# Optimization experiments

Measured on AMD Instinct MI355X. Metric: run time of the kernel, lower is better.

The kernel has to match this reference:

```python
import jax, jax.numpy as jnp
import numpy as np

H_IMG = 128; W_IMG = 128
TANFOVX = 0.5; TANFOVY = 0.5
SCALE_MOD = 1.0
C0 = 0.28209479177387814
C1 = 0.4886025119029199
C2 = (1.0925484305920792, -1.0925484305920792, 0.31539156525252005, -1.0925484305920792, 0.5462742152960396)
C3 = (-0.5900435899266435, 2.890611442640554, -0.4570457994644658, 0.3731763325901154, -0.4570457994644658, 1.445305721320277, -0.5900435899266435)


def quat_to_rot(q):
    q = q / jnp.linalg.norm(q, axis=-1, keepdims=True)
    r, x, y, z = q[..., 0], q[..., 1], q[..., 2], q[..., 3]
    row0 = jnp.stack([1 - 2 * (y * y + z * z), 2 * (x * y - r * z), 2 * (x * z + r * y)], -1)
    row1 = jnp.stack([2 * (x * y + r * z), 1 - 2 * (x * x + z * z), 2 * (y * z - r * x)], -1)
    row2 = jnp.stack([2 * (x * z - r * y), 2 * (y * z + r * x), 1 - 2 * (x * x + y * y)], -1)
    return jnp.stack([row0, row1, row2], -2)  # [P,3,3]


def eval_sh(sh, d):
    # sh: [P,16,3], d: [P,3] unit view directions -> RGB per gaussian (degree 3)
    x, y, z = d[:, 0:1], d[:, 1:2], d[:, 2:3]
    res = C0 * sh[:, 0]
    res = res - C1 * y * sh[:, 1] + C1 * z * sh[:, 2] - C1 * x * sh[:, 3]
    xx, yy, zz = x * x, y * y, z * z
    xy, yz, xz = x * y, y * z, x * z
    res = (res + C2[0] * xy * sh[:, 4] + C2[1] * yz * sh[:, 5]
           + C2[2] * (2 * zz - xx - yy) * sh[:, 6] + C2[3] * xz * sh[:, 7]
           + C2[4] * (xx - yy) * sh[:, 8])
    res = (res + C3[0] * y * (3 * xx - yy) * sh[:, 9] + C3[1] * xy * z * sh[:, 10]
           + C3[2] * y * (4 * zz - xx - yy) * sh[:, 11]
           + C3[3] * z * (2 * zz - 3 * xx - 3 * yy) * sh[:, 12]
           + C3[4] * x * (4 * zz - xx - yy) * sh[:, 13]
           + C3[5] * z * (xx - yy) * sh[:, 14] + C3[6] * x * (xx - 3 * yy) * sh[:, 15])
    return jnp.maximum(res + 0.5, 0.0)


def _render_one(means, sh, opac, scales, rots, bg, target, view, proj, campos):
    P = means.shape[0]
    fx = W_IMG / (2.0 * TANFOVX)
    fy = H_IMG / (2.0 * TANFOVY)
    ones = jnp.ones((P, 1), means.dtype)
    xyz1 = jnp.concatenate([means, ones], axis=1)
    hom = xyz1 @ proj.T                                   # [P,4]
    p_w = 1.0 / (hom[:, 3] + 1e-7)
    p_proj = hom[:, :3] * p_w[:, None]
    p_view = xyz1 @ view.T
    depth = p_view[:, 2]
    in_front = depth > 0.2

    # 3D covariance: Sigma = R diag(s) (R diag(s))^T
    R = quat_to_rot(rots)
    M = R * (scales * SCALE_MOD)[:, None, :]
    Sigma = M @ jnp.swapaxes(M, 1, 2)                     # [P,3,3]

    # EWA Jacobian -> 2D covariance
    tz = depth
    txc = jnp.clip(p_view[:, 0] / tz, -1.3 * TANFOVX, 1.3 * TANFOVX) * tz
    tyc = jnp.clip(p_view[:, 1] / tz, -1.3 * TANFOVY, 1.3 * TANFOVY) * tz
    zp = jnp.zeros_like(tz)
    J = jnp.stack([jnp.stack([fx / tz, zp, -fx * txc / (tz * tz)], -1),
                   jnp.stack([zp, fy / tz, -fy * tyc / (tz * tz)], -1)], -2)  # [P,2,3]
    T = J @ view[:3, :3]
    cov2d = T @ Sigma @ jnp.swapaxes(T, 1, 2)             # [P,2,2]
    c00 = cov2d[:, 0, 0] + 0.3
    c11 = cov2d[:, 1, 1] + 0.3
    c01 = cov2d[:, 0, 1]
    det = c00 * c11 - c01 * c01
    valid = in_front & (det > 1e-12)
    inv_det = 1.0 / jnp.where(det > 1e-12, det, 1.0)
    conic = jnp.stack([c11 * inv_det, -c01 * inv_det, c00 * inv_det], -1)
    mid = 0.5 * (c00 + c11)
    lam = mid + jnp.sqrt(jnp.maximum(mid * mid - det, 0.1))
    radii = jnp.where(valid, jnp.ceil(3.0 * jnp.sqrt(lam)), 0.0)

    # NDC -> pixel centers
    px = ((p_proj[:, 0] + 1.0) * W_IMG - 1.0) * 0.5
    py = ((p_proj[:, 1] + 1.0) * H_IMG - 1.0) * 0.5

    dirs = means - campos[None]
    dirs = dirs / jnp.linalg.norm(dirs, axis=-1, keepdims=True)
    colors = eval_sh(sh, dirs)                            # [P,3]

    # front-to-back depth order (same per-pixel order as the tile sort)
    order = jnp.argsort(depth)
    inv_order = jnp.argsort(order)
    px_s, py_s = px[order], py[order]
    con_s = conic[order]
    col_s = colors[order]
    op_s = opac[order, 0]
    val_s = valid[order]

    xs = jnp.arange(W_IMG, dtype=means.dtype)
    ys = jnp.arange(H_IMG, dtype=means.dtype)
    dx = px_s[:, None, None] - xs[None, None, :]          # [P,1,W] -> [P,H,W]
    dy = py_s[:, None, None] - ys[None, :, None]
    power = (-0.5 * (con_s[:, 0, None, None] * dx * dx + con_s[:, 2, None, None] * dy * dy)
             - con_s[:, 1, None, None] * dx * dy)         # [P,H,W]
    alpha = jnp.minimum(0.99, op_s[:, None, None] * jnp.exp(jnp.minimum(power, 0.0)))
    keep = (power <= 0.0) & (alpha >= 1.0 / 255.0) & val_s[:, None, None]
    alpha = jnp.where(keep, alpha, 0.0)
    trans = jnp.cumprod(1.0 - alpha, axis=0)
    T_exc = jnp.concatenate([jnp.ones((1, H_IMG, W_IMG), alpha.dtype), trans[:-1]], axis=0)
    w = alpha * T_exc                                     # per-gaussian pixel weights
    T_final = trans[-1]
    color = jnp.einsum('phw,pc->chw', w, col_s) + T_final[None] * bg[:, None, None]
    alpha_img = (1.0 - T_final)[None]
    est_color = jnp.einsum('phw,chw->pc', w, target)[inv_order]
    est_weight = w.sum(axis=(1, 2))[inv_order, None]
    return color, alpha_img, est_color, est_weight, radii


def reference(means3D, sh, opacities, scales, rotations, target_image, bg, viewmatrix, projmatrix, campos):
    f = jax.vmap(_render_one, in_axes=(0, 0, 0, 0, 0, 0, 0, None, None, None))
    return f(means3D, sh, opacities, scales, rotations, bg, target_image, viewmatrix, projmatrix, campos)


def setup_inputs() -> dict:
    key = jax.random.key(0)
    ks = jax.random.split(key, 8)
    B, P, K = 2, 1024, 16
    xy = jax.random.normal(ks[0], (B, P, 2), jnp.float32) * 1.5
    z = jax.random.uniform(ks[1], (B, P, 1), jnp.float32, 2.0, 6.0)
    means3D = jnp.concatenate([xy, z], -1)
    sh = jax.random.normal(ks[2], (B, P, K, 3), jnp.float32) * 0.3
    opacities = jax.random.uniform(ks[3], (B, P, 1), jnp.float32)
    scales = jax.random.uniform(ks[4], (B, P, 3), jnp.float32, 0.01, 0.08)
    rotations = jax.random.normal(ks[5], (B, P, 4), jnp.float32)
    target_image = jax.random.uniform(ks[6], (B, 3, H_IMG, W_IMG), jnp.float32)
    bg = jax.random.uniform(ks[7], (B, 3), jnp.float32)
    view = np.eye(4, dtype=np.float32)  # camera at origin, +z forward
    znear, zfar = 0.01, 100.0
    proj = np.zeros((4, 4), np.float32)
    proj[0, 0] = 1.0 / TANFOVX
    proj[1, 1] = 1.0 / TANFOVY
    proj[2, 2] = zfar / (zfar - znear)
    proj[2, 3] = -(zfar * znear) / (zfar - znear)
    proj[3, 2] = 1.0
    return {"means3D": means3D, "sh": sh, "opacities": opacities, "scales": scales,
            "rotations": rotations, "target_image": target_image, "bg": bg,
            "viewmatrix": jnp.asarray(view), "projmatrix": jnp.asarray(proj @ view),
            "campos": jnp.zeros((3,), jnp.float32)}
```

## Files before the change

kernel.cpp:

```cpp
#include <hip/hip_runtime.h>
#include <math.h>

#define HI 128
#define WI 128
#define BB 2
#define PG 1024
#define NE (BB*PG)
#define NTILES 128
#define NRED 16
#define MAGIC_HI 0xFEEDFACECAFE0000ULL
#define MASK_HI  0xFFFFFFFFFFFF0000ULL

#define OFF_ALPHA (BB*3*HI*WI)
#define OFF_ESTC  (OFF_ALPHA + BB*HI*WI)
#define OFF_ESTW  (OFF_ESTC + BB*PG*3)
#define OFF_RADII (OFF_ESTW + BB*PG)

struct PC {
  float px, py, ex, ey;
  float A, B, C, op;
  unsigned key;
  float radii;
};

__device__ __forceinline__ PC proj_cull(int e,
    const float* __restrict__ means, const float* __restrict__ opac,
    const float* __restrict__ scales, const float* __restrict__ rots,
    const float* __restrict__ vm, const float* __restrict__ pm)
{
  PC o;
  float mx = means[e*3+0], my = means[e*3+1], mz = means[e*3+2];

  float hom0 = pm[0]*mx + pm[1]*my + pm[2]*mz + pm[3];
  float hom1 = pm[4]*mx + pm[5]*my + pm[6]*mz + pm[7];
  float hom3 = pm[12]*mx + pm[13]*my + pm[14]*mz + pm[15];
  float p_w  = 1.0f / (hom3 + 1e-7f);
  float pp0 = hom0 * p_w, pp1 = hom1 * p_w;

  float pv0   = vm[0]*mx + vm[1]*my + vm[2]*mz  + vm[3];
  float pv1   = vm[4]*mx + vm[5]*my + vm[6]*mz  + vm[7];
  float depth = vm[8]*mx + vm[9]*my + vm[10]*mz + vm[11];

  float qr = rots[e*4+0], qx = rots[e*4+1], qy = rots[e*4+2], qz = rots[e*4+3];
  float qn = sqrtf(qr*qr + qx*qx + qy*qy + qz*qz);
  qr /= qn; qx /= qn; qy /= qn; qz /= qn;
  float R00 = 1.0f-2.0f*(qy*qy+qz*qz), R01 = 2.0f*(qx*qy-qr*qz), R02 = 2.0f*(qx*qz+qr*qy);
  float R10 = 2.0f*(qx*qy+qr*qz), R11 = 1.0f-2.0f*(qx*qx+qz*qz), R12 = 2.0f*(qy*qz-qr*qx);
  float R20 = 2.0f*(qx*qz-qr*qy), R21 = 2.0f*(qy*qz+qr*qx), R22 = 1.0f-2.0f*(qx*qx+qy*qy);

  float s0 = scales[e*3+0], s1 = scales[e*3+1], s2 = scales[e*3+2];
  float M00=R00*s0, M01=R01*s1, M02=R02*s2;
  float M10=R10*s0, M11=R11*s1, M12=R12*s2;
  float M20=R20*s0, M21=R21*s1, M22=R22*s2;
  float S00 = M00*M00+M01*M01+M02*M02;
  float S01 = M00*M10+M01*M11+M02*M12;
  float S02 = M00*M20+M01*M21+M02*M22;
  float S11 = M10*M10+M11*M11+M12*M12;
  float S12 = M10*M20+M11*M21+M12*M22;
  float S22 = M20*M20+M21*M21+M22*M22;

  const float fx = 128.0f, fyc = 128.0f;
  float tz = depth;
  float txc = fminf(fmaxf(pv0/tz, -0.65f), 0.65f) * tz;
  float tyc = fminf(fmaxf(pv1/tz, -0.65f), 0.65f) * tz;
  float J00 = fx/tz,  J02 = -fx*txc/(tz*tz);
  float J11 = fyc/tz, J12 = -fyc*tyc/(tz*tz);

  float T00 = J00*vm[0] + J02*vm[8];
  float T01 = J00*vm[1] + J02*vm[9];
  float T02 = J00*vm[2] + J02*vm[10];
  float T10 = J11*vm[4] + J12*vm[8];
  float T11 = J11*vm[5] + J12*vm[9];
  float T12 = J11*vm[6] + J12*vm[10];

  float TS00 = T00*S00 + T01*S01 + T02*S02;
  float TS01 = T00*S01 + T01*S11 + T02*S12;
  float TS02 = T00*S02 + T01*S12 + T02*S22;
  float TS10 = T10*S00 + T11*S01 + T12*S02;
  float TS11 = T10*S01 + T11*S11 + T12*S12;
  float TS12 = T10*S02 + T11*S12 + T12*S22;

  float c00 = TS00*T00 + TS01*T01 + TS02*T02 + 0.3f;
  float c01 = TS00*T10 + TS01*T11 + TS02*T12;
  float c11 = TS10*T10 + TS11*T11 + TS12*T12 + 0.3f;

  float det = c00*c11 - c01*c01;
  bool valid = (depth > 0.2f) && (det > 1e-12f);
  float inv_det = 1.0f / (det > 1e-12f ? det : 1.0f);
  o.A =  c11 * inv_det;
  o.B = -c01 * inv_det;
  o.C =  c00 * inv_det;
  float mid = 0.5f * (c00 + c11);
  float lam = mid + sqrtf(fmaxf(mid*mid - det, 0.1f));
  o.radii = valid ? ceilf(3.0f * sqrtf(lam)) : 0.0f;

  o.px = ((pp0 + 1.0f)*WI - 1.0f)*0.5f;
  o.py = ((pp1 + 1.0f)*HI - 1.0f)*0.5f;

  float opv = opac[e];
  o.op = opv;
  float tau = logf(255.0f * opv);
  bool rok = valid && (tau > 0.0f);
  o.ex = rok ? sqrtf(2.0f*tau*c00) + 0.02f : -1e9f;
  o.ey = rok ? sqrtf(2.0f*tau*c11) + 0.02f : -1e9f;

  unsigned u = __float_as_uint(depth);
  o.key = (u >> 31) ? ~u : (u | 0x80000000u);
  return o;
}

__device__ __forceinline__ void sh_color(int e,
    const float* __restrict__ sh, const float* __restrict__ means,
    const float* __restrict__ campos, float col[3])
{
  float mx = means[e*3+0], my = means[e*3+1], mz = means[e*3+2];
  float dxr = mx - campos[0], dyr = my - campos[1], dzr = mz - campos[2];
  float dn = sqrtf(dxr*dxr + dyr*dyr + dzr*dzr);
  float x = dxr/dn, y = dyr/dn, z = dzr/dn;
  float xx=x*x, yy=y*y, zz=z*z, xy=x*y, yz=y*z, xz=x*z;
  const float* S = sh + e*48;
  #pragma unroll
  for (int c = 0; c < 3; ++c) {
    float r = 0.28209479177387814f * S[0+c];
    r -= 0.4886025119029199f * y * S[3+c];
    r += 0.4886025119029199f * z * S[6+c];
    r -= 0.4886025119029199f * x * S[9+c];
    r += 1.0925484305920792f  * xy * S[12+c];
    r += -1.0925484305920792f * yz * S[15+c];
    r += 0.31539156525252005f * (2.0f*zz-xx-yy) * S[18+c];
    r += -1.0925484305920792f * xz * S[21+c];
    r += 0.5462742152960396f  * (xx-yy) * S[24+c];
    r += -0.5900435899266435f * y * (3.0f*xx-yy) * S[27+c];
    r += 2.890611442640554f   * xy * z * S[30+c];
    r += -0.4570457994644658f * y * (4.0f*zz-xx-yy) * S[33+c];
    r += 0.3731763325901154f  * z * (2.0f*zz-3.0f*xx-3.0f*yy) * S[36+c];
    r += -0.4570457994644658f * x * (4.0f*zz-xx-yy) * S[39+c];
    r += 1.445305721320277f   * z * (xx-yy) * S[42+c];
    r += -0.5900435899266435f * x * (xx-3.0f*yy) * S[45+c];
    col[c] = fmaxf(r + 0.5f, 0.0f);
  }
}

__global__ __launch_bounds__(256) void fused_kernel(
    const float* __restrict__ means, const float* __restrict__ sh,
    const float* __restrict__ opac, const float* __restrict__ scales,
    const float* __restrict__ rots, const float* __restrict__ vm,
    const float* __restrict__ pm, const float* __restrict__ campos,
    const float* __restrict__ target, const float* __restrict__ bg,
    float4* __restrict__ pval, unsigned long long* __restrict__ flags,
    int* __restrict__ pgid, float* __restrict__ out)
{
  const int t = threadIdx.x;
  const int blk = blockIdx.x;

  __shared__ unsigned long long skey[PG];
  __shared__ float4 recA[256], recB[256], colC[256], stgt[256];
  __shared__ float  wmat[32][264];
  __shared__ int    scount;
  __shared__ int    scnt[64], soff[65];

  if (blk < NTILES) {
    const int b = blk >> 6, tile = blk & 63;
    const int tx0i = (tile & 7) * 16, ty0i = (tile >> 3) * 16;
    const int xi = tx0i + (t & 15), yi = ty0i + (t >> 4);
    const float fxp = (float)xi, fyp = (float)yi;
    const float rx0 = (float)tx0i, ry0 = (float)ty0i;

    if (t == 0) scount = 0;
    stgt[t] = make_float4(target[((b*3+0)*HI + yi)*WI + xi],
                          target[((b*3+1)*HI + yi)*WI + xi],
                          target[((b*3+2)*HI + yi)*WI + xi], 1.0f);
    __syncthreads();

    for (int k = 0; k < 4; ++k) {
      int ci = k*256 + t;
      PC r = proj_cull((b<<10)+ci, means, opac, scales, rots, vm, pm);
      bool ok = (r.px + r.ex >= rx0) && (r.px - r.ex <= rx0 + 15.0f)
             && (r.py + r.ey >= ry0) && (r.py - r.ey <= ry0 + 15.0f);
      if (ok) {
        int pos = atomicAdd(&scount, 1);
        skey[pos] = (((unsigned long long)r.key) << 10) | (unsigned)ci;
      }
    }
    __syncthreads();
    int total = scount;

    if (total > 1) {
      if (total <= 64) {
        if (t < 64) {
          unsigned long long v = (t < total) ? skey[t] : ~0ull;
          #pragma unroll
          for (int k = 2; k <= 64; k <<= 1) {
            bool dirAsc = ((t & k) == 0);
            #pragma unroll
            for (int j = k >> 1; j > 0; j >>= 1) {
              unsigned long long o = __shfl_xor(v, j, 64);
              bool takeMin = (((t & j) == 0) == dirAsc);
              bool less = v < o;
              v = (takeMin == less) ? v : o;
            }
          }
          if (t < total) skey[t] = v;
        }
        __syncthreads();
      } else {
        int M = 64; while (M < total) M <<= 1;
        for (int i = total + t; i < M; i += 256) skey[i] = ~0ull;
        __syncthreads();
        for (int k = 2; k <= M; k <<= 1)
          for (int j = k >> 1; j > 0; j >>= 1) {
            for (int base = t; base < M; base += 256) {
              int ixj = base ^ j;
              if (ixj > base) {
                unsigned long long a = skey[base], q = skey[ixj];
                bool up = ((base & k) == 0);
                if ((a > q) == up) { skey[base] = q; skey[ixj] = a; }
              }
            }
            __syncthreads();
          }
      }
    }

    float T = 1.0f, a0 = 0.f, a1 = 0.f, a2 = 0.f;

    for (int p0 = 0; p0 < total; p0 += 256) {
      int lim = min(256, total - p0);
      if (p0 + t < total) {
        int gi = (int)(skey[p0 + t] & 1023u);
        int e = (b<<10) + gi;
        PC r = proj_cull(e, means, opac, scales, rots, vm, pm);
        float col[3]; sh_color(e, sh, means, campos, col);
        recA[t] = make_float4(r.px, r.py, r.A, r.B);
        recB[t] = make_float4(r.C, r.op, __int_as_float(gi), 0.f);
        colC[t] = make_float4(col[0], col[1], col[2], 0.f);
      }
      __syncthreads();

      for (int c0 = 0; c0 < lim; c0 += 32) {
        int cc = min(32, lim - c0);
        for (int i = 0; i < cc; ++i) {
          float4 qa = recA[c0+i], qb = recB[c0+i], qc = colC[c0+i];
          float dx = qa.x - fxp, dy = qa.y - fyp;
          float power = -0.5f*(qa.z*dx*dx + qb.x*dy*dy) - qa.w*dx*dy;
          float alpha = fminf(0.99f, qb.y * __expf(power));
          bool keep = (power <= 0.0f) && (alpha >= (1.0f/255.0f));
          float w_ = keep ? alpha * T : 0.0f;
          a0 += w_*qc.x; a1 += w_*qc.y; a2 += w_*qc.z;
          T -= w_;
          wmat[i][t] = w_;
        }
        __syncthreads();
        int row = t >> 3, j = t & 7;
        if (row < cc) {
          float e0=0.f, e1=0.f, e2=0.f, ew=0.f;
          #pragma unroll 8
          for (int k = 0; k < 32; ++k) {
            int p = j + 8*k;
            float w_ = wmat[row][p];
            float4 tg = stgt[p];
            e0 += w_*tg.x; e1 += w_*tg.y; e2 += w_*tg.z; ew += w_;
          }
          #pragma unroll
          for (int o = 4; o; o >>= 1) {
            e0 += __shfl_down(e0, o, 8); e1 += __shfl_down(e1, o, 8);
            e2 += __shfl_down(e2, o, 8); ew += __shfl_down(ew, o, 8);
          }
          if (j == 0) {
            int idx = p0 + c0 + row;
            pgid[blk*PG + idx] = __float_as_int(recB[c0+row].z);
            pval[blk*PG + idx] = make_float4(e0, e1, e2, ew);
          }
        }
        __syncthreads();
      }
    }

    out[((b*3+0)*HI + yi)*WI + xi] = a0 + T * bg[b*3+0];
    out[((b*3+1)*HI + yi)*WI + xi] = a1 + T * bg[b*3+1];
    out[((b*3+2)*HI + yi)*WI + xi] = a2 + T * bg[b*3+2];
    out[OFF_ALPHA + (b*HI + yi)*WI + xi] = 1.0f - T;

    __syncthreads();
    if (t == 0) {
      __threadfence();
      atomicExch(&flags[blk], MAGIC_HI | (unsigned long long)total);
    }
    return;
  }

  const int r = blk - NTILES;
  const int batch = r >> 3, seg = r & 7;

  if (t < 128) {
    int e_own = (batch<<10) + seg*128 + t;
    PC g = proj_cull(e_own, means, opac, scales, rots, vm, pm);
    out[OFF_RADII + e_own] = g.radii;
  }

  float* acc = &wmat[0][0];
  for (int i = t; i < 128*4; i += 256) acc[i] = 0.f;

  if (t < 64) {
    unsigned long long v;
    do { v = atomicAdd(&flags[batch*64 + t], 0ull); }
    while ((v & MASK_HI) != MAGIC_HI);
    scnt[t] = (int)(v & 0xFFFFull);
  }
  __syncthreads();
  __threadfence();

  if (t == 0) {
    int s = 0;
    for (int i = 0; i < 64; ++i) { soff[i] = s; s += scnt[i]; }
    soff[64] = s;
  }
  __syncthreads();
  int E = soff[64];

  for (int idx = t; idx < E; idx += 256) {
    int lo = 0, hi = 63;
    while (lo < hi) { int mid = (lo+hi+1) >> 1; if (soff[mid] <= idx) lo = mid; else hi = mid-1; }
    int tb = batch*64 + lo;
    int j = idx - soff[lo];
    int gi = pgid[tb*PG + j];
    if ((gi >> 7) == seg) {
      float4 v = pval[tb*PG + j];
      int s = gi & 127;
      atomicAdd(&acc[s*4+0], v.x);
      atomicAdd(&acc[s*4+1], v.y);
      atomicAdd(&acc[s*4+2], v.z);
      atomicAdd(&acc[s*4+3], v.w);
    }
  }
  __syncthreads();

  if (t < 128) {
    int e_own = (batch<<10) + seg*128 + t;
    out[OFF_ESTC + e_own*3 + 0] = acc[t*4+0];
    out[OFF_ESTC + e_own*3 + 1] = acc[t*4+1];
    out[OFF_ESTC + e_own*3 + 2] = acc[t*4+2];
    out[OFF_ESTW + e_own]       = acc[t*4+3];
  }
}

extern "C" void kernel_launch(void* const* d_in, const int* in_sizes, int n_in,
                              void* d_out, int out_size, void* d_ws, size_t ws_size,
                              hipStream_t stream) {
  const float* means  = (const float*)d_in[0];
  const float* sh     = (const float*)d_in[1];
  const float* opac   = (const float*)d_in[2];
  const float* scales = (const float*)d_in[3];
  const float* rots   = (const float*)d_in[4];
  const float* target = (const float*)d_in[5];
  const float* bg     = (const float*)d_in[6];
  const float* vm     = (const float*)d_in[7];
  const float* pm     = (const float*)d_in[8];
  const float* campos = (const float*)d_in[9];
  float* out = (float*)d_out;

  float4* pval = (float4*)d_ws;
  unsigned long long* flags = (unsigned long long*)(pval + NTILES*PG);
  int* pgid = (int*)(flags + NTILES);

  fused_kernel<<<NTILES + NRED, 256, 0, stream>>>(
      means, sh, opac, scales, rots, vm, pm, campos, target, bg,
      pval, flags, pgid, out);
}
```

Measured before the change: 21.57 us.

## Use ballot-based wave compaction for culling and split reduction into more blocks

Tile blocks now run a lighter culling routine that skips the inverse-covariance and radii work, and compact visible Gaussians per wave with ballot/popcount instead of shared-memory atomics. A second pass merges the four wave segments into one contiguous key list. The reduction stage uses twice as many blocks, each owning 64 Gaussians, and the spin-wait adds s_sleep to reduce polling pressure. Workspace layout is reordered so flags follow pgid. Risks are the extra sync plus copy pass, and the merge copy reading and writing skey in place, which is safe only if ordering holds.

```diff
diff --git a/kernel.cpp b/kernel.cpp
--- a/kernel.cpp
+++ b/kernel.cpp
@@ -6,10 +6,11 @@
 #define BB 2
 #define PG 1024
 #define NE (BB*PG)
-#define NTILES 128
-#define NRED 16
-#define MAGIC_HI 0xFEEDFACECAFE0000ULL
-#define MASK_HI  0xFFFFFFFFFFFF0000ULL
+#define TPB 64
+#define NTILES (BB*TPB)
+#define NRED 32
+#define MAGIC_HI  0xFEEDFACECAFE0000ULL
+#define MASK_HI   0xFFFFFFFFFFFF0000ULL
 
 #define OFF_ALPHA (BB*3*HI*WI)
 #define OFF_ESTC  (OFF_ALPHA + BB*HI*WI)
@@ -23,69 +24,81 @@
   float radii;
 };
 
+#define PROJ_CORE(e)                                                        \
+  float mx = means[(e)*3+0], my = means[(e)*3+1], mz = means[(e)*3+2];      \
+  float hom0 = pm[0]*mx + pm[1]*my + pm[2]*mz + pm[3];                      \
+  float hom1 = pm[4]*mx + pm[5]*my + pm[6]*mz + pm[7];                      \
+  float hom3 = pm[12]*mx + pm[13]*my + pm[14]*mz + pm[15];                  \
+  float p_w  = 1.0f / (hom3 + 1e-7f);                                       \
+  float pp0 = hom0 * p_w, pp1 = hom1 * p_w;                                 \
+  float pv0   = vm[0]*mx + vm[1]*my + vm[2]*mz  + vm[3];                    \
+  float pv1   = vm[4]*mx + vm[5]*my + vm[6]*mz  + vm[7];                    \
+  float depth = vm[8]*mx + vm[9]*my + vm[10]*mz + vm[11];                   \
+  float qr = rots[(e)*4+0], qx = rots[(e)*4+1], qy = rots[(e)*4+2], qz = rots[(e)*4+3]; \
+  float qn = sqrtf(qr*qr + qx*qx + qy*qy + qz*qz);                          \
+  qr /= qn; qx /= qn; qy /= qn; qz /= qn;                                   \
+  float R00 = 1.0f-2.0f*(qy*qy+qz*qz), R01 = 2.0f*(qx*qy-qr*qz), R02 = 2.0f*(qx*qz+qr*qy); \
+  float R10 = 2.0f*(qx*qy+qr*qz), R11 = 1.0f-2.0f*(qx*qx+qz*qz), R12 = 2.0f*(qy*qz-qr*qx); \
+  float R20 = 2.0f*(qx*qz-qr*qy), R21 = 2.0f*(qy*qz+qr*qx), R22 = 1.0f-2.0f*(qx*qx+qy*qy); \
+  float s0 = scales[(e)*3+0], s1 = scales[(e)*3+1], s2 = scales[(e)*3+2];   \
+  float M00=R00*s0, M01=R01*s1, M02=R02*s2;                                 \
+  float M10=R10*s0, M11=R11*s1, M12=R12*s2;                                 \
+  float M20=R20*s0, M21=R21*s1, M22=R22*s2;                                 \
+  float S00 = M00*M00+M01*M01+M02*M02;                                      \
+  float S01 = M00*M10+M01*M11+M02*M12;                                      \
+  float S02 = M00*M20+M01*M21+M02*M22;                                      \
+  float S11 = M10*M10+M11*M11+M12*M12;                                      \
+  float S12 = M10*M20+M11*M21+M12*M22;                                      \
+  float S22 = M20*M20+M21*M21+M22*M22;                                      \
+  float tz = depth;                                                         \
+  float txc = fminf(fmaxf(pv0/tz, -0.65f), 0.65f) * tz;                     \
+  float tyc = fminf(fmaxf(pv1/tz, -0.65f), 0.65f) * tz;                     \
+  float J00 = 128.0f/tz,  J02 = -128.0f*txc/(tz*tz);                        \
+  float J11 = 128.0f/tz,  J12 = -128.0f*tyc/(tz*tz);                        \
+  float T00 = J00*vm[0] + J02*vm[8];                                        \
+  float T01 = J00*vm[1] + J02*vm[9];                                        \
+  float T02 = J00*vm[2] + J02*vm[10];                                       \
+  float T10 = J11*vm[4] + J12*vm[8];                                        \
+  float T11 = J11*vm[5] + J12*vm[9];                                        \
+  float T12 = J11*vm[6] + J12*vm[10];                                       \
+  float TS00 = T00*S00 + T01*S01 + T02*S02;                                 \
+  float TS01 = T00*S01 + T01*S11 + T02*S12;                                 \
+  float TS02 = T00*S02 + T01*S12 + T02*S22;                                 \
+  float TS10 = T10*S00 + T11*S01 + T12*S02;                                 \
+  float TS11 = T10*S01 + T11*S11 + T12*S12;                                 \
+  float TS12 = T10*S02 + T11*S12 + T12*S22;                                 \
+  float c00 = TS00*T00 + TS01*T01 + TS02*T02 + 0.3f;                        \
+  float c01 = TS00*T10 + TS01*T11 + TS02*T12;                               \
+  float c11 = TS10*T10 + TS11*T11 + TS12*T12 + 0.3f;                        \
+  float det = c00*c11 - c01*c01;                                            \
+  bool valid = (depth > 0.2f) && (det > 1e-12f);                            \
+  float opv = opac[(e)];                                                    \
+  float tau = logf(255.0f * opv);                                           \
+  bool rok = valid && (tau > 0.0f);
+
+__device__ __forceinline__ void cull_lite(int e,
+    const float* __restrict__ means, const float* __restrict__ opac,
+    const float* __restrict__ scales, const float* __restrict__ rots,
+    const float* __restrict__ vm, const float* __restrict__ pm,
+    float& px, float& py, float& ex, float& ey, unsigned& key)
+{
+  PROJ_CORE(e)
+  px = ((pp0 + 1.0f)*WI - 1.0f)*0.5f;
+  py = ((pp1 + 1.0f)*HI - 1.0f)*0.5f;
+  ex = rok ? sqrtf(2.0f*tau*c00) + 0.02f : -1e9f;
+  ey = rok ? sqrtf(2.0f*tau*c11) + 0.02f : -1e9f;
+  unsigned u = __float_as_uint(depth);
+  key = (u >> 31) ? ~u : (u | 0x80000000u);
+  (void)valid; (void)opv; (void)c01; (void)det;
+}
+
 __device__ __forceinline__ PC proj_cull(int e,
     const float* __restrict__ means, const float* __restrict__ opac,
     const float* __restrict__ scales, const float* __restrict__ rots,
     const float* __restrict__ vm, const float* __restrict__ pm)
 {
   PC o;
-  float mx = means[e*3+0], my = means[e*3+1], mz = means[e*3+2];
-
-  float hom0 = pm[0]*mx + pm[1]*my + pm[2]*mz + pm[3];
-  float hom1 = pm[4]*mx + pm[5]*my + pm[6]*mz + pm[7];
-  float hom3 = pm[12]*mx + pm[13]*my + pm[14]*mz + pm[15];
-  float p_w  = 1.0f / (hom3 + 1e-7f);
-  float pp0 = hom0 * p_w, pp1 = hom1 * p_w;
-
-  float pv0   = vm[0]*mx + vm[1]*my + vm[2]*mz  + vm[3];
-  float pv1   = vm[4]*mx + vm[5]*my + vm[6]*mz  + vm[7];
-  float depth = vm[8]*mx + vm[9]*my + vm[10]*mz + vm[11];
-
-  float qr = rots[e*4+0], qx = rots[e*4+1], qy = rots[e*4+2], qz = rots[e*4+3];
-  float qn = sqrtf(qr*qr + qx*qx + qy*qy + qz*qz);
-  qr /= qn; qx /= qn; qy /= qn; qz /= qn;
-  float R00 = 1.0f-2.0f*(qy*qy+qz*qz), R01 = 2.0f*(qx*qy-qr*qz), R02 = 2.0f*(qx*qz+qr*qy);
-  float R10 = 2.0f*(qx*qy+qr*qz), R11 = 1.0f-2.0f*(qx*qx+qz*qz), R12 = 2.0f*(qy*qz-qr*qx);
-  float R20 = 2.0f*(qx*qz-qr*qy), R21 = 2.0f*(qy*qz+qr*qx), R22 = 1.0f-2.0f*(qx*qx+qy*qy);
-
-  float s0 = scales[e*3+0], s1 = scales[e*3+1], s2 = scales[e*3+2];
-  float M00=R00*s0, M01=R01*s1, M02=R02*s2;
-  float M10=R10*s0, M11=R11*s1, M12=R12*s2;
-  float M20=R20*s0, M21=R21*s1, M22=R22*s2;
-  float S00 = M00*M00+M01*M01+M02*M02;
-  float S01 = M00*M10+M01*M11+M02*M12;
-  float S02 = M00*M20+M01*M21+M02*M22;
-  float S11 = M10*M10+M11*M11+M12*M12;
-  float S12 = M10*M20+M11*M21+M12*M22;
-  float S22 = M20*M20+M21*M21+M22*M22;
-
-  const float fx = 128.0f, fyc = 128.0f;
-  float tz = depth;
-  float txc = fminf(fmaxf(pv0/tz, -0.65f), 0.65f) * tz;
-  float tyc = fminf(fmaxf(pv1/tz, -0.65f), 0.65f) * tz;
-  float J00 = fx/tz,  J02 = -fx*txc/(tz*tz);
-  float J11 = fyc/tz, J12 = -fyc*tyc/(tz*tz);
-
-  float T00 = J00*vm[0] + J02*vm[8];
-  float T01 = J00*vm[1] + J02*vm[9];
-  float T02 = J00*vm[2] + J02*vm[10];
-  float T10 = J11*vm[4] + J12*vm[8];
-  float T11 = J11*vm[5] + J12*vm[9];
-  float T12 = J11*vm[6] + J12*vm[10];
-
-  float TS00 = T00*S00 + T01*S01 + T02*S02;
-  float TS01 = T00*S01 + T01*S11 + T02*S12;
-  float TS02 = T00*S02 + T01*S12 + T02*S22;
-  float TS10 = T10*S00 + T11*S01 + T12*S02;
-  float TS11 = T10*S01 + T11*S11 + T12*S12;
-  float TS12 = T10*S02 + T11*S12 + T12*S22;
-
-  float c00 = TS00*T00 + TS01*T01 + TS02*T02 + 0.3f;
-  float c01 = TS00*T10 + TS01*T11 + TS02*T12;
-  float c11 = TS10*T10 + TS11*T11 + TS12*T12 + 0.3f;
-
-  float det = c00*c11 - c01*c01;
-  bool valid = (depth > 0.2f) && (det > 1e-12f);
+  PROJ_CORE(e)
   float inv_det = 1.0f / (det > 1e-12f ? det : 1.0f);
   o.A =  c11 * inv_det;
   o.B = -c01 * inv_det;
@@ -93,17 +106,11 @@
   float mid = 0.5f * (c00 + c11);
   float lam = mid + sqrtf(fmaxf(mid*mid - det, 0.1f));
   o.radii = valid ? ceilf(3.0f * sqrtf(lam)) : 0.0f;
-
   o.px = ((pp0 + 1.0f)*WI - 1.0f)*0.5f;
   o.py = ((pp1 + 1.0f)*HI - 1.0f)*0.5f;
-
-  float opv = opac[e];
   o.op = opv;
-  float tau = logf(255.0f * opv);
-  bool rok = valid && (tau > 0.0f);
   o.ex = rok ? sqrtf(2.0f*tau*c00) + 0.02f : -1e9f;
   o.ey = rok ? sqrtf(2.0f*tau*c11) + 0.02f : -1e9f;
-
   unsigned u = __float_as_uint(depth);
   o.key = (u >> 31) ? ~u : (u | 0x80000000u);
   return o;
@@ -147,16 +154,18 @@
     const float* __restrict__ rots, const float* __restrict__ vm,
     const float* __restrict__ pm, const float* __restrict__ campos,
     const float* __restrict__ target, const float* __restrict__ bg,
-    float4* __restrict__ pval, unsigned long long* __restrict__ flags,
-    int* __restrict__ pgid, float* __restrict__ out)
+    float4* __restrict__ pval, int* __restrict__ pgid,
+    unsigned long long* __restrict__ tileflags,
+    float* __restrict__ out)
 {
   const int t = threadIdx.x;
+  const int wv = t >> 6, ln = t & 63;
   const int blk = blockIdx.x;
 
   __shared__ unsigned long long skey[PG];
   __shared__ float4 recA[256], recB[256], colC[256], stgt[256];
   __shared__ float  wmat[32][264];
-  __shared__ int    scount;
+  __shared__ int    wcnt[4];
   __shared__ int    scnt[64], soff[65];
 
   if (blk < NTILES) {
@@ -166,24 +175,37 @@
     const float fxp = (float)xi, fyp = (float)yi;
     const float rx0 = (float)tx0i, ry0 = (float)ty0i;
 
-    if (t == 0) scount = 0;
     stgt[t] = make_float4(target[((b*3+0)*HI + yi)*WI + xi],
                           target[((b*3+1)*HI + yi)*WI + xi],
                           target[((b*3+2)*HI + yi)*WI + xi], 1.0f);
+
+    int cnt = 0;
+    unsigned long long kbuf[4]; int kok = 0;
+    for (int k = 0; k < 4; ++k) {
+      int ci = wv*256 + k*64 + ln;
+      float px, py, ex, ey; unsigned key;
+      cull_lite((b<<10)+ci, means, opac, scales, rots, vm, pm, px, py, ex, ey, key);
+      bool ok = (px + ex >= rx0) && (px - ex <= rx0 + 15.0f)
+             && (py + ey >= ry0) && (py - ey <= ry0 + 15.0f);
+      unsigned long long m = __ballot(ok);
+      if (ok) {
+        kbuf[kok] = (((unsigned long long)key) << 10) | (unsigned)ci;
+        int pos = cnt + __popcll(m & ((1ull << ln) - 1ull));
+        skey[wv*256 + pos] = kbuf[kok];
+        ++kok;
+      }
+      cnt += __popcll(m);
+    }
+    if (ln == 0) wcnt[wv] = cnt;
     __syncthreads();
-
-    for (int k = 0; k < 4; ++k) {
-      int ci = k*256 + t;
-      PC r = proj_cull((b<<10)+ci, means, opac, scales, rots, vm, pm);
-      bool ok = (r.px + r.ex >= rx0) && (r.px - r.ex <= rx0 + 15.0f)
-             && (r.py + r.ey >= ry0) && (r.py - r.ey <= ry0 + 15.0f);
-      if (ok) {
-        int pos = atomicAdd(&scount, 1);
-        skey[pos] = (((unsigned long long)r.key) << 10) | (unsigned)ci;
-      }
+    int c0_ = wcnt[0], c1_ = wcnt[1], c2_ = wcnt[2], c3_ = wcnt[3];
+    int total = c0_ + c1_ + c2_ + c3_;
+    int off = (wv>0?c0_:0) + (wv>1?c1_:0) + (wv>2?c2_:0);
+    for (int i = ln; i < cnt; i += 64) {
+      unsigned long long v = skey[wv*256 + i];
+      skey[off + i] = v;
     }
     __syncthreads();
-    int total = scount;
 
     if (total > 1) {
       if (total <= 64) {
@@ -284,27 +306,28 @@
     __syncthreads();
     if (t == 0) {
       __threadfence();
-      atomicExch(&flags[blk], MAGIC_HI | (unsigned long long)total);
+      atomicExch(&tileflags[blk], MAGIC_HI | (unsigned long long)total);
     }
     return;
   }
 
   const int r = blk - NTILES;
-  const int batch = r >> 3, seg = r & 7;
-
-  if (t < 128) {
-    int e_own = (batch<<10) + seg*128 + t;
+  const int batch = r >> 4, seg = r & 15;
+
+  if (t < 64) {
+    int e_own = (batch<<10) + seg*64 + t;
     PC g = proj_cull(e_own, means, opac, scales, rots, vm, pm);
     out[OFF_RADII + e_own] = g.radii;
   }
 
   float* acc = &wmat[0][0];
-  for (int i = t; i < 128*4; i += 256) acc[i] = 0.f;
+  for (int i = t; i < 64*4; i += 256) acc[i] = 0.f;
 
   if (t < 64) {
     unsigned long long v;
-    do { v = atomicAdd(&flags[batch*64 + t], 0ull); }
-    while ((v & MASK_HI) != MAGIC_HI);
+    do { v = atomicAdd(&tileflags[batch*TPB + t], 0ull);
+         if ((v & MASK_HI) != MAGIC_HI) __builtin_amdgcn_s_sleep(2);
+    } while ((v & MASK_HI) != MAGIC_HI);
     scnt[t] = (int)(v & 0xFFFFull);
   }
   __syncthreads();
@@ -312,21 +335,21 @@
 
   if (t == 0) {
     int s = 0;
-    for (int i = 0; i < 64; ++i) { soff[i] = s; s += scnt[i]; }
-    soff[64] = s;
+    for (int i = 0; i < TPB; ++i) { soff[i] = s; s += scnt[i]; }
+    soff[TPB] = s;
   }
   __syncthreads();
-  int E = soff[64];
+  int E = soff[TPB];
 
   for (int idx = t; idx < E; idx += 256) {
-    int lo = 0, hi = 63;
+    int lo = 0, hi = TPB-1;
     while (lo < hi) { int mid = (lo+hi+1) >> 1; if (soff[mid] <= idx) lo = mid; else hi = mid-1; }
-    int tb = batch*64 + lo;
+    int tb = batch*TPB + lo;
     int j = idx - soff[lo];
     int gi = pgid[tb*PG + j];
-    if ((gi >> 7) == seg) {
+    if ((gi >> 6) == seg) {
       float4 v = pval[tb*PG + j];
-      int s = gi & 127;
+      int s = gi & 63;
       atomicAdd(&acc[s*4+0], v.x);
       atomicAdd(&acc[s*4+1], v.y);
       atomicAdd(&acc[s*4+2], v.z);
@@ -335,8 +358,8 @@
   }
   __syncthreads();
 
-  if (t < 128) {
-    int e_own = (batch<<10) + seg*128 + t;
+  if (t < 64) {
+    int e_own = (batch<<10) + seg*64 + t;
     out[OFF_ESTC + e_own*3 + 0] = acc[t*4+0];
     out[OFF_ESTC + e_own*3 + 1] = acc[t*4+1];
     out[OFF_ESTC + e_own*3 + 2] = acc[t*4+2];
@@ -360,10 +383,10 @@
   float* out = (float*)d_out;
 
   float4* pval = (float4*)d_ws;
-  unsigned long long* flags = (unsigned long long*)(pval + NTILES*PG);
-  int* pgid = (int*)(flags + NTILES);
+  int* pgid = (int*)(pval + NTILES*PG);
+  unsigned long long* tileflags = (unsigned long long*)(pgid + NTILES*PG);
 
   fused_kernel<<<NTILES + NRED, 256, 0, stream>>>(
       means, sh, opac, scales, rots, vm, pm, campos, target, bg,
-      pval, flags, pgid, out);
-}
+      pval, pgid, tileflags, out);
+}
```

After: 22.70 us. 5.3% more time.
